# Kernel tuning notes

Measured on AMD Instinct MI355X. Metric: run time of the kernel, lower is better.

The kernel has to match this reference:

```python
import jax, jax.numpy as jnp
import numpy as np

B, R, T, D = 16, 1024, 512, 1024
H = 1024  # hidden_dim

def setup_inputs() -> dict:
    key = jax.random.key(0)
    ks = jax.random.split(key, 8)
    s_in = 1.0 / np.sqrt(D)
    s_comb = 1.0 / np.sqrt(3 * D)
    return {
        "region_feats": jax.random.normal(ks[0], (B, R, D), jnp.float32),
        "query_embs": jax.random.normal(ks[1], (B, T, D), jnp.float32),
        "Wr": jax.random.normal(ks[2], (D, H), jnp.float32) * s_in,
        "br": jnp.zeros((H,), jnp.float32),
        "Wq": jax.random.normal(ks[3], (D, H), jnp.float32) * s_in,
        "bq": jnp.zeros((H,), jnp.float32),
        "Ws": jax.random.normal(ks[4], (3 * D, 1), jnp.float32) * s_comb,
        "bs": jnp.zeros((1,), jnp.float32),
    }

def reference(region_feats, query_embs, Wr, br, Wq, bq, Ws, bs):
    # Dense projections
    R_proj = region_feats @ Wr + br            # [B,R,H]
    Q_proj = query_embs @ Wq + bq              # [B,T,H]
    # Unscaled cross-attention scores
    scores = jnp.einsum('brd,btd->brt', R_proj, Q_proj)  # [B,R,T]
    attn = jax.nn.softmax(scores, axis=-1)
    # Attend over RAW query embeddings (as in source)
    attended = jnp.einsum('brt,btd->brd', attn, query_embs)  # [B,R,D]
    combined = jnp.concatenate(
        [region_feats, attended, region_feats * attended], axis=-1)  # [B,R,3D]
    out = combined @ Ws + bs                    # [B,R,1]
    return jnp.squeeze(out, axis=-1)            # [B,R]
```

## Files before the change

### kernel.cpp

```cpp
#include <hip/hip_runtime.h>


#define BD 16
#define RD 1024
#define TD 512
#define DD 1024
#define BR (BD * RD)

typedef _Float16 half8 __attribute__((ext_vector_type(8)));
typedef _Float16 half4 __attribute__((ext_vector_type(4)));
typedef float floatx4 __attribute__((ext_vector_type(4)));

__device__ __forceinline__ float wave_sum(float v) {
#pragma unroll
  for (int off = 32; off > 0; off >>= 1) v += __shfl_down(v, off);
  return v;
}

__device__ __forceinline__ half8 cvt8(float4 a, float4 b) {
  half8 h = {(_Float16)a.x, (_Float16)a.y, (_Float16)a.z, (_Float16)a.w,
             (_Float16)b.x, (_Float16)b.y, (_Float16)b.z, (_Float16)b.w};
  return h;
}

__device__ __forceinline__ void gl16(const _Float16* g, _Float16* l) {
  __builtin_amdgcn_global_load_lds(
      (const __attribute__((address_space(1))) void*)g,
      (__attribute__((address_space(3))) void*)l, 16, 0, 0);
}

__global__ __launch_bounds__(256) void prep_all(
    const float* __restrict__ Wr, const float* __restrict__ Wq,
    const float* __restrict__ Ws, const float* __restrict__ br,
    const float* __restrict__ region, const float* __restrict__ query,
    _Float16* __restrict__ M2, _Float16* __restrict__ Ws16,
    float* __restrict__ wqbr, _Float16* __restrict__ wqbr16,
    _Float16* __restrict__ r16, float* __restrict__ rdvec,
    _Float16* __restrict__ q16, float* __restrict__ h1) {
  __shared__ __align__(16) _Float16 lds[2 * 2 * 2048];
  const int blk = blockIdx.x, tid = threadIdx.x;

  if (blk < 256) {
    const int m0 = (blk >> 4) * 64, n0 = (blk & 15) * 64;
    const int lane = tid & 63, w = tid >> 6;
    const int wr = w >> 1, wc = w & 1;
    const int srow = tid >> 2, slot = tid & 3;
    const int scol = (slot ^ ((srow >> 1) & 3)) * 8;
    const long offA = (long)(m0 + srow) * DD + scol;
    const long offB = (long)(n0 + srow) * DD + scol;
    const int wofs = srow * 32 + slot * 8;
    const int NK = DD / 32;
    float4 a0, a1, b0, b1;
    a0 = *(const float4*)(Wr + offA); a1 = *(const float4*)(Wr + offA + 4);
    b0 = *(const float4*)(Wq + offB); b1 = *(const float4*)(Wq + offB + 4);
    *(int4*)&lds[wofs] = *(int4*)&(const half8&)cvt8(a0, a1);
    {
      half8 hb = cvt8(b0, b1);
      *(half8*)&lds[2048 + wofs] = hb;
    }
    a0 = *(const float4*)(Wr + offA + 32); a1 = *(const float4*)(Wr + offA + 36);
    b0 = *(const float4*)(Wq + offB + 32); b1 = *(const float4*)(Wq + offB + 36);
    __syncthreads();
    floatx4 acc[2][2] = {};
    const int fr = lane & 15, g = lane >> 4;
    const int fs = (g ^ ((fr >> 1) & 3)) * 8;
    for (int kt = 0; kt < NK; ++kt) {
      const int cur = (kt & 1) * 4096, nxt = ((kt + 1) & 1) * 4096;
      if (kt + 1 < NK) {
        half8 ha = cvt8(a0, a1), hb = cvt8(b0, b1);
        *(half8*)&lds[nxt + wofs] = ha;
        *(half8*)&lds[nxt + 2048 + wofs] = hb;
      }
      if (kt + 2 < NK) {
        const long go = (long)(kt + 2) * 32;
        a0 = *(const float4*)(Wr + offA + go); a1 = *(const float4*)(Wr + offA + go + 4);
        b0 = *(const float4*)(Wq + offB + go); b1 = *(const float4*)(Wq + offB + go + 4);
      }
      half8 af[2], bf[2];
#pragma unroll
      for (int i = 0; i < 2; ++i)
        af[i] = *(const half8*)&lds[cur + (32 * wr + 16 * i + fr) * 32 + fs];
#pragma unroll
      for (int j = 0; j < 2; ++j)
        bf[j] = *(const half8*)&lds[cur + 2048 + (32 * wc + 16 * j + fr) * 32 + fs];
#pragma unroll
      for (int i = 0; i < 2; ++i)
#pragma unroll
        for (int j = 0; j < 2; ++j)
          acc[i][j] = __builtin_amdgcn_mfma_f32_16x16x32_f16(af[i], bf[j], acc[i][j], 0, 0, 0);
      __syncthreads();
    }
    const int cr = g * 4, cc = fr;
#pragma unroll
    for (int i = 0; i < 2; ++i)
#pragma unroll
      for (int r = 0; r < 4; ++r)
#pragma unroll
        for (int j = 0; j < 2; ++j)
          M2[(long)(m0 + 32 * wr + 16 * i + cr + r) * DD + n0 + 32 * wc + 16 * j + cc] =
              (_Float16)acc[i][j][r];
  } else if (blk < 258) {
    const long i = (long)(blk - 256) * 1024 + tid * 4;
    const float4 v = *(const float4*)&Ws[DD + i];
    half4 h = {(_Float16)v.x, (_Float16)v.y, (_Float16)v.z, (_Float16)v.w};
    *(half4*)&Ws16[i] = h;
  } else if (blk < 514) {
    const int row = (blk - 258) * 4 + (tid >> 6);
    const int lane = tid & 63;
    const float* x = Wq + (long)row * DD;
    float s = 0.f;
    for (int k = lane; k < DD; k += 64) s += x[k] * br[k];
    s = wave_sum(s);
    if (lane == 0) {
      wqbr[row] = s;
      wqbr16[row] = (_Float16)s;
    }
  } else if (blk < 514 + BR / 4) {
    const int wid = tid >> 6, lane = tid & 63;
    const long row = (long)(blk - 514) * 4 + wid;
    const float* src = region + row * DD;
    _Float16* dst = r16 + row * DD;
    float rd = 0.f;
#pragma unroll
    for (int it = 0; it < 4; ++it) {
      const int c = it * 256 + lane * 4;
      const float4 v = *(const float4*)&src[c];
      const float4 w0 = *(const float4*)&Ws[c];
      half4 h = {(_Float16)v.x, (_Float16)v.y, (_Float16)v.z, (_Float16)v.w};
      *(half4*)&dst[c] = h;
      rd += v.x * w0.x + v.y * w0.y + v.z * w0.z + v.w * w0.w;
    }
    rd = wave_sum(rd);
    if (lane == 0) rdvec[row] = rd;
  } else {
    const int wid = tid >> 6, lane = tid & 63;
    const long row = (long)(blk - (514 + BR / 4)) * 4 + wid;
    const float* src = query + row * DD;
    _Float16* dst = q16 + row * DD;
    float hq = 0.f;
#pragma unroll
    for (int it = 0; it < 4; ++it) {
      const int c = it * 256 + lane * 4;
      const float4 v = *(const float4*)&src[c];
      const float4 w1 = *(const float4*)&Ws[DD + c];
      half4 h = {(_Float16)v.x, (_Float16)v.y, (_Float16)v.z, (_Float16)v.w};
      *(half4*)&dst[c] = h;
      hq += v.x * w1.x + v.y * w1.y + v.z * w1.z + v.w * w1.w;
    }
    hq = wave_sum(hq);
    if (lane == 0) h1[row] = hq;
  }
}

__global__ __launch_bounds__(512, 4) void qp_gemm(
    const _Float16* __restrict__ A, const _Float16* __restrict__ B,
    _Float16* __restrict__ C, const _Float16* __restrict__ wq16,
    float* __restrict__ cvec) {
  __shared__ __align__(16) _Float16 lds[2 * 2 * 4096];
  const int lin = blockIdx.x;
  const int s = lin & 7, u = lin >> 3;
  const int mt = s * 8 + (u >> 3), nt = u & 7;
  const int m0 = mt * 128, n0 = nt * 128;
  const int tid = threadIdx.x, lane = tid & 63, w = tid >> 6;
  const int wr = w >> 1, wc = w & 1;

  const int lrow = lane >> 2, slot = lane & 3;
  const int scol = (slot ^ ((lrow >> 1) & 3)) * 8;
  const int srow = 16 * w + lrow;
  const _Float16* gA = A + (long)(m0 + srow) * DD + scol;
  const _Float16* gB = B + (long)(n0 + srow) * DD + scol;
  const int wbase = 512 * w;

  gl16(gA, &lds[wbase]);
  gl16(gB, &lds[4096 + wbase]);
  __syncthreads();

  floatx4 acc[2][4] = {};
  float cvp[2] = {0.f, 0.f};
  const int fr = lane & 15, g = lane >> 4;
  const int fs = (g ^ ((fr >> 1) & 3)) * 8;
  const int NK = DD / 32;

  for (int kt = 0; kt < NK; ++kt) {
    const int cur = (kt & 1) * 8192, nxt = cur ^ 8192;
    if (kt + 1 < NK) {
      const long go = (long)(kt + 1) * 32;
      gl16(gA + go, &lds[nxt + wbase]);
      gl16(gB + go, &lds[nxt + 4096 + wbase]);
    }
    half8 af[2], bf[4];
#pragma unroll
    for (int i = 0; i < 2; ++i)
      af[i] = *(const half8*)&lds[cur + (32 * wr + 16 * i + fr) * 32 + fs];
#pragma unroll
    for (int j = 0; j < 4; ++j)
      bf[j] = *(const half8*)&lds[cur + 4096 + (64 * wc + 16 * j + fr) * 32 + fs];
    if (wc == 0) {
      const half8 wb = *(const half8*)&wq16[kt * 32 + g * 8];
#pragma unroll
      for (int i = 0; i < 2; ++i)
#pragma unroll
        for (int e = 0; e < 8; ++e)
          cvp[i] += (float)af[i][e] * (float)wb[e];
    }
#pragma unroll
    for (int i = 0; i < 2; ++i)
#pragma unroll
      for (int j = 0; j < 4; ++j)
        acc[i][j] = __builtin_amdgcn_mfma_f32_16x16x32_f16(af[i], bf[j], acc[i][j], 0, 0, 0);
    __syncthreads();
  }

  if (wc == 0 && nt == 0) {
#pragma unroll
    for (int i = 0; i < 2; ++i) {
      float c = cvp[i];
      c += __shfl_xor(c, 16);
      c += __shfl_xor(c, 32);
      if (lane < 16) cvec[m0 + 32 * wr + 16 * i + lane] = c;
    }
  }

  const int cr = g * 4, cc = fr;
#pragma unroll
  for (int i = 0; i < 2; ++i)
#pragma unroll
    for (int r = 0; r < 4; ++r)
#pragma unroll
      for (int j = 0; j < 4; ++j)
        C[(long)(m0 + 32 * wr + 16 * i + cr + r) * DD + n0 + 64 * wc + 16 * j + cc] =
            (_Float16)acc[i][j][r];
}

#define STAGE3(hh, sl)                                    \
  {                                                       \
    const long go_ = (long)(hh) * 32;                     \
    gl16(gA + go_, &lds[(sl) * 12288 + wbase]);           \
    gl16(gP + go_, &lds[(sl) * 12288 + 4096 + wbase]);    \
    gl16(gQ + go_, &lds[(sl) * 12288 + 8192 + wbase]);    \
  }

#define HALFSTEP(h, sl, VM)                                                    \
  {                                                                            \
    asm volatile("s_waitcnt vmcnt(" #VM ")" ::: "memory");                     \
    __builtin_amdgcn_s_barrier();                                              \
    asm volatile("" ::: "memory");                                             \
    half8 af[4], bp[2], bq[2];                                                 \
    _Pragma("unroll") for (int i = 0; i < 4; ++i)                              \
      af[i] = *(const half8*)&lds[(sl) * 12288 + (64 * wr + 16 * i + fr) * 32 + fs]; \
    _Pragma("unroll") for (int j = 0; j < 2; ++j)                              \
      bp[j] = *(const half8*)&lds[(sl) * 12288 + 4096 + (32 * wc + 16 * j + fr) * 32 + fs]; \
    _Pragma("unroll") for (int j = 0; j < 2; ++j)                              \
      bq[j] = *(const half8*)&lds[(sl) * 12288 + 8192 + (32 * wc + 16 * j + fr) * 32 + fs]; \
    const half8 w2f = *(const half8*)&wlds[(h) * 32 + g * 8];                  \
    bq[0] *= w2f;                                                              \
    bq[1] *= w2f;                                                              \
    __builtin_amdgcn_s_setprio(1);                                             \
    _Pragma("unroll") for (int i = 0; i < 4; ++i)                              \
      _Pragma("unroll") for (int j = 0; j < 2; ++j)                            \
        accS[i][j] = __builtin_amdgcn_mfma_f32_16x16x32_f16(af[i], bp[j], accS[i][j], 0, 0, 0); \
    _Pragma("unroll") for (int i = 0; i < 4; ++i)                              \
      _Pragma("unroll") for (int j = 0; j < 2; ++j)                            \
        accH[i][j] = __builtin_amdgcn_mfma_f32_16x16x32_f16(af[i], bq[j], accH[i][j], 0, 0, 0); \
    __builtin_amdgcn_s_setprio(0);                                             \
    __builtin_amdgcn_s_barrier();                                              \
    asm volatile("" ::: "memory");                                             \
  }

__global__ __launch_bounds__(512, 2) void gemm_fused(
    const _Float16* __restrict__ A, const _Float16* __restrict__ B0,
    const _Float16* __restrict__ B1,
    float* __restrict__ Ms, float* __restrict__ Ls, float* __restrict__ Hs,
    const float* __restrict__ cvec, const float* __restrict__ h1,
    const _Float16* __restrict__ wsh, long sA, long sB) {
  __shared__ __align__(16) _Float16 lds[4 * 12288];
  __shared__ __align__(16) _Float16 wlds[1024];

  const int lin = blockIdx.x;
  const int s = lin & 7, u = lin >> 3;
  const int b = 2 * s + (u >> 5);
  const int t = u & 31;
  const int mt = t >> 2, nt = t & 3;
  const int m0 = mt * 128, n0 = nt * 128;
  A += (long)b * sA;
  B0 += (long)b * sB;
  B1 += (long)b * sB;

  const int tid = threadIdx.x, lane = tid & 63, w = tid >> 6;
  const int wr = w >> 2, wc = w & 3;

  const int lrow = lane >> 2, slot = lane & 3;
  const int scol = (slot ^ ((lrow >> 1) & 3)) * 8;
  const int srow = 16 * w + lrow;
  const _Float16* gA = A + (long)(m0 + srow) * DD + scol;
  const _Float16* gP = B0 + (long)(n0 + srow) * DD + scol;
  const _Float16* gQ = B1 + (long)(n0 + srow) * DD + scol;
  const int wbase = 512 * w;

  if (tid < 128) *(int4*)&wlds[tid * 8] = *(const int4*)&wsh[1024 + tid * 8];
  __syncthreads();

  floatx4 accS[4][2] = {};
  floatx4 accH[4][2] = {};
  const int fr = lane & 15, g = lane >> 4;
  const int fs = (g ^ ((fr >> 1) & 3)) * 8;

  STAGE3(0, 0);
  STAGE3(1, 1);
  STAGE3(2, 2);

  for (int hb = 0; hb < 28; hb += 4) {
    STAGE3(hb + 3, 3); HALFSTEP(hb + 0, 0, 9);
    STAGE3(hb + 4, 0); HALFSTEP(hb + 1, 1, 9);
    STAGE3(hb + 5, 1); HALFSTEP(hb + 2, 2, 9);
    STAGE3(hb + 6, 2); HALFSTEP(hb + 3, 3, 9);
  }
  STAGE3(31, 3); HALFSTEP(28, 0, 9);
  HALFSTEP(29, 1, 6);
  HALFSTEP(30, 2, 3);
  HALFSTEP(31, 3, 0);

  const int cr = g * 4, cc = fr;
  float cv[2], hv[2];
#pragma unroll
  for (int j = 0; j < 2; ++j) {
    const long col = (long)b * TD + n0 + 32 * wc + 16 * j + cc;
    cv[j] = cvec[col];
    hv[j] = h1[col];
  }
  const int chunk = nt * 4 + wc;
  const long rowBase = (long)b * RD + m0 + 64 * wr + cr;
#pragma unroll
  for (int i = 0; i < 4; ++i) {
#pragma unroll
    for (int r = 0; r < 4; ++r) {
      float mx = fmaxf(accS[i][0][r] + cv[0], accS[i][1][r] + cv[1]);
      mx = fmaxf(mx, __shfl_xor(mx, 1));
      mx = fmaxf(mx, __shfl_xor(mx, 2));
      mx = fmaxf(mx, __shfl_xor(mx, 4));
      mx = fmaxf(mx, __shfl_xor(mx, 8));
      float l = 0.f, hs = 0.f;
#pragma unroll
      for (int j = 0; j < 2; ++j) {
        const float e = __expf(accS[i][j][r] + cv[j] - mx);
        l += e;
        hs += e * (accH[i][j][r] + hv[j]);
      }
      l += __shfl_xor(l, 1); hs += __shfl_xor(hs, 1);
      l += __shfl_xor(l, 2); hs += __shfl_xor(hs, 2);
      l += __shfl_xor(l, 4); hs += __shfl_xor(hs, 4);
      l += __shfl_xor(l, 8); hs += __shfl_xor(hs, 8);
      if (cc == 0) {
        const long idx = (long)chunk * BR + rowBase + 16 * i + r;
        Ms[idx] = mx;
        Ls[idx] = l;
        Hs[idx] = hs;
      }
    }
  }
}

__global__ __launch_bounds__(256) void combine(
    const float* __restrict__ Ms, const float* __restrict__ Ls,
    const float* __restrict__ Hs, const float* __restrict__ rdvec,
    const float* __restrict__ bs, float* __restrict__ out) {
  const int row = blockIdx.x * 256 + threadIdx.x;
  float mv[16];
  float gm = -1e30f;
#pragma unroll
  for (int c = 0; c < 16; ++c) {
    mv[c] = Ms[(long)c * BR + row];
    gm = fmaxf(gm, mv[c]);
  }
  float L = 0.f, HS = 0.f;
#pragma unroll
  for (int c = 0; c < 16; ++c) {
    const float sc = __expf(mv[c] - gm);
    L += Ls[(long)c * BR + row] * sc;
    HS += Hs[(long)c * BR + row] * sc;
  }
  out[row] = HS / L + rdvec[row] + bs[0];
}

extern "C" void kernel_launch(void* const* d_in, const int* in_sizes, int n_in,
                              void* d_out, int out_size, void* d_ws, size_t ws_size,
                              hipStream_t stream) {
  const float* region = (const float*)d_in[0];
  const float* query  = (const float*)d_in[1];
  const float* Wr     = (const float*)d_in[2];
  const float* br     = (const float*)d_in[3];
  const float* Wq     = (const float*)d_in[4];
  const float* Ws     = (const float*)d_in[6];
  const float* bs     = (const float*)d_in[7];
  float* out = (float*)d_out;

  char* p = (char*)d_ws;
  _Float16* region16 = (_Float16*)p;
  _Float16* query16  = (_Float16*)(p + (32u << 20));
  _Float16* Qp       = (_Float16*)(p + (48u << 20));
  _Float16* M2       = (_Float16*)(p + (64u << 20));
  _Float16* Ws16     = (_Float16*)(p + (66u << 20));
  float*    wqbr     = (float*)(p + (66u << 20) + 8192);
  _Float16* wqbr16   = (_Float16*)(p + (66u << 20) + 12288);
  float*    cvec     = (float*)(p + (66u << 20) + 16384);
  float*    rdvec    = (float*)(p + (66u << 20) + 65536);
  float*    h1       = (float*)(p + (66u << 20) + 131072);
  float*    Ms       = (float*)(p + (67u << 20));
  float*    Ls       = Ms + 16 * BR;
  float*    Hs       = Ls + 16 * BR;

  prep_all<<<dim3(514 + BR / 4 + BD * TD / 4), 256, 0, stream>>>(
      Wr, Wq, Ws, br, region, query, M2, Ws16, wqbr, wqbr16,
      region16, rdvec, query16, h1);
  qp_gemm<<<dim3(512), 512, 0, stream>>>(query16, M2, Qp, wqbr16, cvec);
  gemm_fused<<<dim3(512), 512, 0, stream>>>(
      region16, Qp, query16, Ms, Ls, Hs, cvec, h1, Ws16,
      (long)RD * DD, (long)TD * DD);
  combine<<<dim3(BR / 256), 256, 0, stream>>>(Ms, Ls, Hs, rdvec, bs, out);
}
```

Baseline: 227.3 us.

## Deepen qp_gemm prefetch pipeline and trim gemm_fused to 3 stages, one barrier

qp_gemm moves from a 2-buffer loop with a full syncthreads per k-step to a 4-slot global_load_lds pipeline. It uses explicit vmcnt waits and a single barrier per step, and stages the Wq vector in LDS. gemm_fused drops from 4 to 3 LDS stages, replaces the two barriers per step with one, and raises its launch-bounds occupancy hint to 4. The goal is to hide global-load latency and cut barrier stalls. In exchange, qp_gemm's LDS per block roughly doubles, which can lower its resident blocks per CU. The 128-register cap from the new hint in gemm_fused may also cause spills.

```diff
diff --git a/kernel.cpp b/kernel.cpp
--- a/kernel.cpp
+++ b/kernel.cpp
@@ -28,6 +28,12 @@
       (const __attribute__((address_space(1))) void*)g,
       (__attribute__((address_space(3))) void*)l, 16, 0, 0);
 }
+
+#define VMW_(N) asm volatile("s_waitcnt vmcnt(" #N ")" ::: "memory")
+#define VMW(N) VMW_(N)
+#define BARR                        \
+  __builtin_amdgcn_s_barrier();     \
+  asm volatile("" ::: "memory")
 
 __global__ __launch_bounds__(256) void prep_all(
     const float* __restrict__ Wr, const float* __restrict__ Wq,
@@ -152,11 +158,39 @@
   }
 }
 
+#define STAGE2(hh, sl)                                  \
+  {                                                     \
+    const long go_ = (long)(hh) * 32;                   \
+    gl16(gA + go_, &lds[(sl) * 8192 + wbase]);          \
+    gl16(gB + go_, &lds[(sl) * 8192 + 4096 + wbase]);   \
+  }
+
+#define COMP2(h, sl)                                                           \
+  {                                                                            \
+    half8 af[2], bf[4];                                                        \
+    _Pragma("unroll") for (int i = 0; i < 2; ++i)                              \
+      af[i] = *(const half8*)&lds[(sl) * 8192 + (32 * wr + 16 * i + fr) * 32 + fs]; \
+    _Pragma("unroll") for (int j = 0; j < 4; ++j)                              \
+      bf[j] = *(const half8*)&lds[(sl) * 8192 + 4096 + (64 * wc + 16 * j + fr) * 32 + fs]; \
+    if (wc == 0) {                                                             \
+      const half8 wb = *(const half8*)&wq_lds[(h) * 32 + g * 8];               \
+      _Pragma("unroll") for (int i = 0; i < 2; ++i)                            \
+        _Pragma("unroll") for (int e = 0; e < 8; ++e)                          \
+          cvp[i] += (float)af[i][e] * (float)wb[e];                            \
+    }                                                                          \
+    __builtin_amdgcn_s_setprio(1);                                             \
+    _Pragma("unroll") for (int i = 0; i < 2; ++i)                              \
+      _Pragma("unroll") for (int j = 0; j < 4; ++j)                            \
+        acc[i][j] = __builtin_amdgcn_mfma_f32_16x16x32_f16(af[i], bf[j], acc[i][j], 0, 0, 0); \
+    __builtin_amdgcn_s_setprio(0);                                             \
+  }
+
 __global__ __launch_bounds__(512, 4) void qp_gemm(
     const _Float16* __restrict__ A, const _Float16* __restrict__ B,
     _Float16* __restrict__ C, const _Float16* __restrict__ wq16,
     float* __restrict__ cvec) {
-  __shared__ __align__(16) _Float16 lds[2 * 2 * 4096];
+  __shared__ __align__(16) _Float16 lds[4 * 8192];
+  __shared__ __align__(16) _Float16 wq_lds[1024];
   const int lin = blockIdx.x;
   const int s = lin & 7, u = lin >> 3;
   const int mt = s * 8 + (u >> 3), nt = u & 7;
@@ -171,45 +205,27 @@
   const _Float16* gB = B + (long)(n0 + srow) * DD + scol;
   const int wbase = 512 * w;
 
-  gl16(gA, &lds[wbase]);
-  gl16(gB, &lds[4096 + wbase]);
+  if (tid < 128) *(int4*)&wq_lds[tid * 8] = *(const int4*)&wq16[tid * 8];
   __syncthreads();
 
   floatx4 acc[2][4] = {};
   float cvp[2] = {0.f, 0.f};
   const int fr = lane & 15, g = lane >> 4;
   const int fs = (g ^ ((fr >> 1) & 3)) * 8;
-  const int NK = DD / 32;
-
-  for (int kt = 0; kt < NK; ++kt) {
-    const int cur = (kt & 1) * 8192, nxt = cur ^ 8192;
-    if (kt + 1 < NK) {
-      const long go = (long)(kt + 1) * 32;
-      gl16(gA + go, &lds[nxt + wbase]);
-      gl16(gB + go, &lds[nxt + 4096 + wbase]);
-    }
-    half8 af[2], bf[4];
-#pragma unroll
-    for (int i = 0; i < 2; ++i)
-      af[i] = *(const half8*)&lds[cur + (32 * wr + 16 * i + fr) * 32 + fs];
-#pragma unroll
-    for (int j = 0; j < 4; ++j)
-      bf[j] = *(const half8*)&lds[cur + 4096 + (64 * wc + 16 * j + fr) * 32 + fs];
-    if (wc == 0) {
-      const half8 wb = *(const half8*)&wq16[kt * 32 + g * 8];
-#pragma unroll
-      for (int i = 0; i < 2; ++i)
-#pragma unroll
-        for (int e = 0; e < 8; ++e)
-          cvp[i] += (float)af[i][e] * (float)wb[e];
-    }
-#pragma unroll
-    for (int i = 0; i < 2; ++i)
-#pragma unroll
-      for (int j = 0; j < 4; ++j)
-        acc[i][j] = __builtin_amdgcn_mfma_f32_16x16x32_f16(af[i], bf[j], acc[i][j], 0, 0, 0);
-    __syncthreads();
-  }
+
+  STAGE2(0, 0); STAGE2(1, 1); STAGE2(2, 2);
+  VMW(4); BARR;
+
+  for (int hb = 0; hb < 28; hb += 4) {
+    STAGE2(hb + 3, 3); COMP2(hb + 0, 0); VMW(4); BARR;
+    STAGE2(hb + 4, 0); COMP2(hb + 1, 1); VMW(4); BARR;
+    STAGE2(hb + 5, 1); COMP2(hb + 2, 2); VMW(4); BARR;
+    STAGE2(hb + 6, 2); COMP2(hb + 3, 3); VMW(4); BARR;
+  }
+  STAGE2(31, 3); COMP2(28, 0); VMW(4); BARR;
+  COMP2(29, 1); VMW(2); BARR;
+  COMP2(30, 2); VMW(0); BARR;
+  COMP2(31, 3);
 
   if (wc == 0 && nt == 0) {
 #pragma unroll
@@ -240,11 +256,8 @@
     gl16(gQ + go_, &lds[(sl) * 12288 + 8192 + wbase]);    \
   }
 
-#define HALFSTEP(h, sl, VM)                                                    \
+#define COMP3(h, sl)                                                           \
   {                                                                            \
-    asm volatile("s_waitcnt vmcnt(" #VM ")" ::: "memory");                     \
-    __builtin_amdgcn_s_barrier();                                              \
-    asm volatile("" ::: "memory");                                             \
     half8 af[4], bp[2], bq[2];                                                 \
     _Pragma("unroll") for (int i = 0; i < 4; ++i)                              \
       af[i] = *(const half8*)&lds[(sl) * 12288 + (64 * wr + 16 * i + fr) * 32 + fs]; \
@@ -263,17 +276,15 @@
       _Pragma("unroll") for (int j = 0; j < 2; ++j)                            \
         accH[i][j] = __builtin_amdgcn_mfma_f32_16x16x32_f16(af[i], bq[j], accH[i][j], 0, 0, 0); \
     __builtin_amdgcn_s_setprio(0);                                             \
-    __builtin_amdgcn_s_barrier();                                              \
-    asm volatile("" ::: "memory");                                             \
-  }
-
-__global__ __launch_bounds__(512, 2) void gemm_fused(
+  }
+
+__global__ __launch_bounds__(512, 4) void gemm_fused(
     const _Float16* __restrict__ A, const _Float16* __restrict__ B0,
     const _Float16* __restrict__ B1,
     float* __restrict__ Ms, float* __restrict__ Ls, float* __restrict__ Hs,
     const float* __restrict__ cvec, const float* __restrict__ h1,
     const _Float16* __restrict__ wsh, long sA, long sB) {
-  __shared__ __align__(16) _Float16 lds[4 * 12288];
+  __shared__ __align__(16) _Float16 lds[3 * 12288];
   __shared__ __align__(16) _Float16 wlds[1024];
 
   const int lin = blockIdx.x;
@@ -305,20 +316,16 @@
   const int fr = lane & 15, g = lane >> 4;
   const int fs = (g ^ ((fr >> 1) & 3)) * 8;
 
-  STAGE3(0, 0);
-  STAGE3(1, 1);
-  STAGE3(2, 2);
-
-  for (int hb = 0; hb < 28; hb += 4) {
-    STAGE3(hb + 3, 3); HALFSTEP(hb + 0, 0, 9);
-    STAGE3(hb + 4, 0); HALFSTEP(hb + 1, 1, 9);
-    STAGE3(hb + 5, 1); HALFSTEP(hb + 2, 2, 9);
-    STAGE3(hb + 6, 2); HALFSTEP(hb + 3, 3, 9);
-  }
-  STAGE3(31, 3); HALFSTEP(28, 0, 9);
-  HALFSTEP(29, 1, 6);
-  HALFSTEP(30, 2, 3);
-  HALFSTEP(31, 3, 0);
+  STAGE3(0, 0); STAGE3(1, 1);
+  VMW(3); BARR;
+
+  for (int hb = 0; hb < 30; hb += 3) {
+    STAGE3(hb + 2, 2); COMP3(hb + 0, 0); VMW(3); BARR;
+    STAGE3(hb + 3, 0); COMP3(hb + 1, 1); VMW(3); BARR;
+    STAGE3(hb + 4, 1); COMP3(hb + 2, 2); VMW(3); BARR;
+  }
+  COMP3(30, 0); VMW(0); BARR;
+  COMP3(31, 1);
 
   const int cr = g * 4, cc = fr;
   float cv[2], hv[2];
```

Result: faster. 216.5 us (-4.7%).
